# Kernel optimization log

Measured on AMD Instinct MI355X. Metric: run time of the kernel, lower is better.

The kernel has to match this reference:

```python
import jax, jax.numpy as jnp
import numpy as np

D_MODEL = 1024
HEADS = 16
HEAD_DIM = D_MODEL // HEADS


def setup_inputs() -> dict:
    key = jax.random.key(0)
    ks = jax.random.split(key, 6)
    B, S, D = 2, 2048, D_MODEL
    scale = 1.0 / np.sqrt(D)
    x = jax.random.normal(ks[0], (B, S, D), dtype=jnp.float32)
    mask = jax.random.randint(ks[1], (B, S), 0, 2, dtype=jnp.int32)
    Wq = jax.random.normal(ks[2], (D, D), dtype=jnp.float32) * scale
    Wk = jax.random.normal(ks[3], (D, D), dtype=jnp.float32) * scale
    Wv = jax.random.normal(ks[4], (D, D), dtype=jnp.float32) * scale
    Wp = jax.random.normal(ks[5], (D, D), dtype=jnp.float32) * scale
    zb = jnp.zeros((D,), dtype=jnp.float32)
    return {"x": x, "mask": mask, "Wq": Wq, "bq": zb, "Wk": Wk, "bk": zb,
            "Wv": Wv, "bv": zb, "Wp": Wp, "bp": zb}


def reference(x, mask, Wq, bq, Wk, bk, Wv, bv, Wp, bp):
    B, S, D = x.shape
    H, Dh = HEADS, HEAD_DIM

    def split_heads(t):  # [B,S,D] -> [B,H,S,Dh]
        return t.reshape(B, S, H, Dh).transpose(0, 2, 1, 3)

    q = split_heads(x @ Wq + bq)
    k = split_heads(x @ Wk + bk)
    v = split_heads(x @ Wv + bv)

    att = jnp.einsum('bhqd,bhkd->bhqk', q, k) / jnp.sqrt(jnp.float32(Dh))
    # key-padding mask: [B,S] -> [B,1,1,S]; masked positions -> -inf
    m = (mask[:, None, None, :] != 0)
    att = jnp.where(m, att, -jnp.inf)
    att = jax.nn.softmax(att, axis=-1)
    # rows that were fully masked produce NaN -> zero them (masked_fill(isnan, 0))
    att = jnp.where(jnp.isnan(att), 0.0, att)

    y = jnp.einsum('bhqk,bhkd->bhqd', att, v)  # [B,H,S,Dh]
    y = y.transpose(0, 2, 1, 3).reshape(B, S, D)
    return y @ Wp + bp
```

## Files before the change

kernel.cpp:

```cpp
#include <hip/hip_runtime.h>
#include <math.h>

#define D_MODEL 1024
#define HEADS 16
#define HEAD_DIM 64
#define SEQ 2048
#define BATCH 2
#define KVT 64
#define QTILE 128
#define SCALE_Q 0.18033688f

typedef __attribute__((ext_vector_type(8))) short bf16x8;
typedef __attribute__((ext_vector_type(4))) float f32x4;

__device__ __forceinline__ short f2bf(float f) {
    union { float f; unsigned u; } v; v.f = f;
    unsigned r = (v.u + 0x7FFFu + ((v.u >> 16) & 1u)) >> 16;
    return (short)r;
}

__device__ __forceinline__ unsigned cvt_pk_bf16(float lo, float hi) {
    unsigned r;
    asm("v_cvt_pk_bf16_f32 %0, %1, %2" : "=v"(r) : "v"(lo), "v"(hi));
    return r;
}

__device__ __forceinline__ float fexp2(float x) {
    float r;
    asm("v_exp_f32 %0, %1" : "=v"(r) : "v"(x));
    return r;
}

__global__ __launch_bounds__(256) void prep(
    const float* __restrict__ x, const float* __restrict__ Wq,
    const float* __restrict__ Wk, const float* __restrict__ Wv,
    const float* __restrict__ Wp, const int* __restrict__ mask,
    short* __restrict__ xb, short* __restrict__ Wqkvt,
    short* __restrict__ Wpt, float* __restrict__ maskf) {
    __shared__ float t[32][33];
    const int bid = blockIdx.x;
    if (bid < 2048) {
        const int i = bid * 256 + threadIdx.x;
        float4 a = ((const float4*)x)[2 * i];
        float4 b = ((const float4*)x)[2 * i + 1];
        short r[8] = {f2bf(a.x), f2bf(a.y), f2bf(a.z), f2bf(a.w),
                      f2bf(b.x), f2bf(b.y), f2bf(b.z), f2bf(b.w)};
        *(uint4*)(xb + 8 * i) = *(uint4*)r;
    } else if (bid < 6144) {
        const int tt = bid - 2048;
        const int z = tt >> 10;
        const int rem = tt & 1023;
        const float* W = z == 0 ? Wq : z == 1 ? Wk : z == 2 ? Wv : Wp;
        short* dst = (z < 3) ? Wqkvt + (size_t)z * 1024 * 1024 : Wpt;
        const int n0 = (rem & 31) * 32, k0 = (rem >> 5) * 32;
        const int tx = threadIdx.x & 31, ty = threadIdx.x >> 5;
#pragma unroll
        for (int j = 0; j < 4; ++j)
            t[ty + j * 8][tx] = W[(size_t)(k0 + ty + j * 8) * 1024 + n0 + tx];
        __syncthreads();
#pragma unroll
        for (int j = 0; j < 4; ++j) {
            const int n = ty + j * 8;
            dst[(size_t)(n0 + n) * 1024 + k0 + tx] = f2bf(t[tx][n]);
        }
    } else {
        const int i = (bid - 6144) * 256 + threadIdx.x;
        maskf[i] = mask[i] ? 0.f : -INFINITY;
    }
}

template <int MODE>
__global__ __launch_bounds__(256) void mfma_gemm(
    const short* __restrict__ A, const short* __restrict__ Bt,
    const float* __restrict__ b0, const float* __restrict__ b1,
    const float* __restrict__ b2, float* __restrict__ outf,
    short* __restrict__ o0, short* __restrict__ o1, short* __restrict__ o2,
    int M, int N, int K) {
    __shared__ short As[2 * 128 * 32];
    __shared__ short Bs[2 * 128 * 32];

    const int tid = threadIdx.x;
    const int wave = tid >> 6, lane = tid & 63;
    const int l15 = lane & 15, lhi = lane >> 4;
    const int wm = wave >> 1, wn = wave & 1;

    const int nwgx = gridDim.x;
    const int nwg = nwgx * gridDim.y;
    const int lin = blockIdx.y * nwgx + blockIdx.x;
    const int swz = (lin & 7) * (nwg >> 3) + (lin >> 3);
    const int bm0 = (swz / nwgx) * 128, bn0 = (swz % nwgx) * 128;

    f32x4 acc[4][4];
#pragma unroll
    for (int m = 0; m < 4; ++m)
#pragma unroll
        for (int n = 0; n < 4; ++n) acc[m][n] = (f32x4){0.f, 0.f, 0.f, 0.f};

#define STAGE_G(buf, kt_)                                                         \
    {                                                                             \
        const int k0 = (kt_) * 32;                                                \
        _Pragma("unroll") for (int p = 0; p < 2; ++p) {                           \
            const int o = (wave * 2 + p) * 64 + lane;                             \
            const int r = o >> 2;                                                 \
            const int gs = (o & 3) ^ ((r >> 1) & 3);                              \
            __builtin_amdgcn_global_load_lds(                                     \
                (const __attribute__((address_space(1))) void*)(                  \
                    A + (size_t)(bm0 + r) * K + k0 + gs * 8),                     \
                (__attribute__((address_space(3))) void*)(                        \
                    As + (size_t)(buf) * 4096 + (wave * 2 + p) * 512),            \
                16, 0, 0);                                                        \
            __builtin_amdgcn_global_load_lds(                                     \
                (const __attribute__((address_space(1))) void*)(                  \
                    Bt + (size_t)(bn0 + r) * K + k0 + gs * 8),                    \
                (__attribute__((address_space(3))) void*)(                        \
                    Bs + (size_t)(buf) * 4096 + (wave * 2 + p) * 512),            \
                16, 0, 0);                                                        \
        }                                                                         \
    }

    const int NT = K / 32;
    STAGE_G(0, 0);
    __syncthreads();
    for (int kt = 0; kt < NT; ++kt) {
        const int cur = kt & 1;
        if (kt + 1 < NT) STAGE_G((kt + 1) & 1, kt + 1);
        bf16x8 af[4], bf[4];
        const int sg = (lhi ^ ((l15 >> 1) & 3)) * 16;
#pragma unroll
        for (int m = 0; m < 4; ++m)
            af[m] = *(const bf16x8*)((char*)As + cur * 8192 +
                                     (wm * 64 + m * 16 + l15) * 64 + sg);
#pragma unroll
        for (int n = 0; n < 4; ++n)
            bf[n] = *(const bf16x8*)((char*)Bs + cur * 8192 +
                                     (wn * 64 + n * 16 + l15) * 64 + sg);
        __builtin_amdgcn_s_setprio(1);
#pragma unroll
        for (int m = 0; m < 4; ++m)
#pragma unroll
            for (int n = 0; n < 4; ++n)
                acc[m][n] = __builtin_amdgcn_mfma_f32_16x16x32_bf16(af[m], bf[n], acc[m][n], 0, 0, 0);
        __builtin_amdgcn_s_setprio(0);
        __syncthreads();
    }
#undef STAGE_G

    const int which = (MODE == 1) ? (bn0 >> 10) : 0;
#pragma unroll
    for (int m = 0; m < 4; ++m) {
#pragma unroll
        for (int n = 0; n < 4; ++n) {
            const int col = bn0 + wn * 64 + n * 16 + l15;
            if (MODE == 0) {
#pragma unroll
                for (int rr = 0; rr < 4; ++rr) {
                    const int row = bm0 + wm * 64 + m * 16 + lhi * 4 + rr;
                    outf[(size_t)row * N + col] = acc[m][n][rr] + b0[col];
                }
            } else {
                const int cc = col & 1023;
                const int h = cc >> 6, dh = cc & 63;
                const int row0 = bm0 + wm * 64 + m * 16 + lhi * 4;
                const int b = row0 >> 11, s0 = row0 & (SEQ - 1);
                if (which == 2) {
                    const float bias = b2[cc];
                    uint2 w;
                    w.x = cvt_pk_bf16(acc[m][n][0] + bias, acc[m][n][1] + bias);
                    w.y = cvt_pk_bf16(acc[m][n][2] + bias, acc[m][n][3] + bias);
                    *(uint2*)(o2 + ((size_t)(b * HEADS + h) * HEAD_DIM + dh) * SEQ + s0) = w;
                } else {
                    const float bias = (which == 0 ? b0 : b1)[cc];
                    short* dst = which == 0 ? o0 : o1;
#pragma unroll
                    for (int rr = 0; rr < 4; ++rr) {
                        float v = acc[m][n][rr] + bias;
                        if (which == 0) v *= SCALE_Q;
                        dst[(((size_t)(b * HEADS + h)) * SEQ + s0 + rr) * HEAD_DIM + dh] = f2bf(v);
                    }
                }
            }
        }
    }
}

__global__ __launch_bounds__(256, 2) void flash_attn(
    const short* __restrict__ Q, const short* __restrict__ K,
    const short* __restrict__ Vt, const float* __restrict__ maskf,
    short* __restrict__ Y) {
    __shared__ unsigned char kt[2][KVT * 128];
    __shared__ unsigned char vt[2][HEAD_DIM * 128];
    __shared__ unsigned char pb[4][32 * 128];

    const int tid = threadIdx.x;
    const int wave = tid >> 6;
    const int lane = tid & 63;
    const int l15 = lane & 15;
    const int lhi = lane >> 4;

    const int nwg = gridDim.x;
    const int wg = blockIdx.x;
    const int swz = (wg & 7) * (nwg >> 3) + (wg >> 3);
    const int qt = swz & 15;
    const int bh = swz >> 4;
    const int b = bh >> 4;

    const int q0 = qt * QTILE + wave * 32;

    bf16x8 qf[2][2];
#pragma unroll
    for (int qi = 0; qi < 2; ++qi) {
        const short* Qp = Q + ((size_t)bh * SEQ + q0 + 16 * qi + l15) * HEAD_DIM;
        qf[qi][0] = *(const bf16x8*)(Qp + 8 * lhi);
        qf[qi][1] = *(const bf16x8*)(Qp + 8 * lhi + 32);
    }

    const unsigned char* Kb8 = (const unsigned char*)(K + (size_t)bh * SEQ * HEAD_DIM);
    const unsigned char* Vb8 = (const unsigned char*)(Vt + (size_t)bh * HEAD_DIM * SEQ);
    const float* mb = maskf + b * SEQ;

#define STAGE(buf, kvi)                                                            \
    {                                                                              \
        const unsigned char* kbase = Kb8 + (size_t)(kvi) * KVT * 128;              \
        const unsigned char* vbase = Vb8 + (size_t)(kvi) * 128;                    \
        _Pragma("unroll") for (int p = 0; p < 2; ++p) {                            \
            const int o = (wave * 2 + p) * 64 + lane;                              \
            const int row = o >> 3;                                                \
            const int inner = (o & 7) * 16;                                        \
            const int src = inner ^ ((row & 7) << 4);                              \
            __builtin_amdgcn_global_load_lds(                                      \
                (const __attribute__((address_space(1))) void*)(                   \
                    kbase + row * 128 + src),                                      \
                (__attribute__((address_space(3))) void*)(                         \
                    &kt[buf][(wave * 2 + p) * 1024]),                              \
                16, 0, 0);                                                         \
            __builtin_amdgcn_global_load_lds(                                      \
                (const __attribute__((address_space(1))) void*)(                   \
                    vbase + (size_t)row * (SEQ * 2) + src),                        \
                (__attribute__((address_space(3))) void*)(                         \
                    &vt[buf][(wave * 2 + p) * 1024]),                              \
                16, 0, 0);                                                         \
        }                                                                          \
    }

    f32x4 accO[2][4];
    float lrow[2] = {0.f, 0.f};
#pragma unroll
    for (int qi = 0; qi < 2; ++qi)
#pragma unroll
        for (int i = 0; i < 4; ++i) accO[qi][i] = (f32x4){0.f, 0.f, 0.f, 0.f};

    STAGE(0, 0);
    __syncthreads();

    for (int kv = 0; kv < SEQ / KVT; ++kv) {
        const int cur = kv & 1;
        if (kv + 1 < SEQ / KVT) STAGE((kv + 1) & 1, kv + 1);

        const int k0 = kv * KVT;

        f32x4 accS[2][4];
#pragma unroll
        for (int qi = 0; qi < 2; ++qi)
#pragma unroll
            for (int nt = 0; nt < 4; ++nt) accS[qi][nt] = (f32x4){0.f, 0.f, 0.f, 0.f};
#pragma unroll
        for (int c = 0; c < 2; ++c) {
            bf16x8 kf[4];
#pragma unroll
            for (int nt = 0; nt < 4; ++nt) {
                const int key = l15 + 16 * nt;
                kf[nt] = *(const bf16x8*)(kt[cur] + key * 128 +
                                          ((16 * lhi + 64 * c) ^ ((key & 7) << 4)));
            }
            __builtin_amdgcn_s_setprio(1);
#pragma unroll
            for (int qi = 0; qi < 2; ++qi)
#pragma unroll
                for (int nt = 0; nt < 4; ++nt)
                    accS[qi][nt] = __builtin_amdgcn_mfma_f32_16x16x32_bf16(
                        kf[nt], qf[qi][c], accS[qi][nt], 0, 0, 0);
            __builtin_amdgcn_s_setprio(0);
        }

        f32x4 ma[4];
#pragma unroll
        for (int nt = 0; nt < 4; ++nt)
            ma[nt] = *(const f32x4*)(mb + k0 + 16 * nt + 4 * lhi);

#pragma unroll
        for (int qi = 0; qi < 2; ++qi) {
#pragma unroll
            for (int nt = 0; nt < 4; ++nt) {
                f32x4 p;
#pragma unroll
                for (int r = 0; r < 4; ++r) {
                    p[r] = fexp2(accS[qi][nt][r] + ma[nt][r]);
                    lrow[qi] += p[r];
                }
                uint2 w;
                w.x = cvt_pk_bf16(p[0], p[1]);
                w.y = cvt_pk_bf16(p[2], p[3]);
                *(uint2*)(pb[wave] + (l15 + 16 * qi) * 128 +
                          ((32 * nt + 8 * lhi) ^ (l15 << 3))) = w;
            }
        }

#pragma unroll
        for (int c = 0; c < 2; ++c) {
            bf16x8 pf[2];
#pragma unroll
            for (int qi = 0; qi < 2; ++qi) {
                union { bf16x8 v; uint2 u[2]; } pfu;
                pfu.u[0] = *(const uint2*)(pb[wave] + (l15 + 16 * qi) * 128 +
                                           ((16 * lhi + 64 * c) ^ (l15 << 3)));
                pfu.u[1] = *(const uint2*)(pb[wave] + (l15 + 16 * qi) * 128 +
                                           ((16 * lhi + 64 * c + 8) ^ (l15 << 3)));
                pf[qi] = pfu.v;
            }
            bf16x8 vf[4];
#pragma unroll
            for (int d = 0; d < 4; ++d) {
                const int dh = l15 + 16 * d;
                vf[d] = *(const bf16x8*)(vt[cur] + dh * 128 +
                                         ((16 * lhi + 64 * c) ^ ((dh & 7) << 4)));
            }
            __builtin_amdgcn_s_setprio(1);
#pragma unroll
            for (int qi = 0; qi < 2; ++qi)
#pragma unroll
                for (int d = 0; d < 4; ++d)
                    accO[qi][d] = __builtin_amdgcn_mfma_f32_16x16x32_bf16(
                        vf[d], pf[qi], accO[qi][d], 0, 0, 0);
            __builtin_amdgcn_s_setprio(0);
        }
        __syncthreads();
    }
#undef STAGE

#pragma unroll
    for (int qi = 0; qi < 2; ++qi) {
        float rs = lrow[qi];
        rs += __shfl_xor(rs, 16);
        rs += __shfl_xor(rs, 32);
        const float inv = (rs > 0.f) ? 1.f / rs : 0.f;
        const int qg = q0 + 16 * qi + l15;
        short* Yp = Y + ((size_t)b * SEQ + qg) * D_MODEL + (bh & 15) * HEAD_DIM;
#pragma unroll
        for (int d = 0; d < 4; ++d) {
            uint2 w;
            w.x = cvt_pk_bf16(accO[qi][d][0] * inv, accO[qi][d][1] * inv);
            w.y = cvt_pk_bf16(accO[qi][d][2] * inv, accO[qi][d][3] * inv);
            *(uint2*)(Yp + 16 * d + 4 * lhi) = w;
        }
    }
}

extern "C" void kernel_launch(void* const* d_in, const int* in_sizes, int n_in,
                              void* d_out, int out_size, void* d_ws, size_t ws_size,
                              hipStream_t stream) {
    const float* x    = (const float*)d_in[0];
    const int*   mask = (const int*)  d_in[1];
    const float* Wq   = (const float*)d_in[2];
    const float* bq   = (const float*)d_in[3];
    const float* Wk   = (const float*)d_in[4];
    const float* bk   = (const float*)d_in[5];
    const float* Wv   = (const float*)d_in[6];
    const float* bv   = (const float*)d_in[7];
    const float* Wp   = (const float*)d_in[8];
    const float* bp   = (const float*)d_in[9];
    float* out = (float*)d_out;

    short* ws    = (short*)d_ws;
    short* xb    = ws;
    short* Wqkvt = xb + ((size_t)4 << 20);
    short* Wpt   = Wqkvt + ((size_t)3 << 20);
    short* Qb    = Wpt + ((size_t)1 << 20);
    short* Kb    = Qb + ((size_t)4 << 20);
    short* Vtb   = Kb + ((size_t)4 << 20);
    short* Yb    = Vtb + ((size_t)4 << 20);
    float* maskf = (float*)(Yb + ((size_t)4 << 20));

    const int M = BATCH * SEQ;

    prep<<<dim3(6160), 256, 0, stream>>>(x, Wq, Wk, Wv, Wp, mask,
                                         xb, Wqkvt, Wpt, maskf);

    mfma_gemm<1><<<dim3(3 * D_MODEL / 128, M / 128), 256, 0, stream>>>(
        xb, Wqkvt, bq, bk, bv, nullptr, Qb, Kb, Vtb, M, 3 * D_MODEL, D_MODEL);

    flash_attn<<<dim3(BATCH * HEADS * (SEQ / QTILE)), 256, 0, stream>>>(Qb, Kb, Vtb, maskf, Yb);

    mfma_gemm<0><<<dim3(D_MODEL / 128, M / 128), 256, 0, stream>>>(
        Yb, Wpt, bp, bp, bp, out, nullptr, nullptr, nullptr, M, D_MODEL, D_MODEL);
}
```

Before: 123.7 us.

## Split attention KV range in two and merge partial outputs in a new kernel

Splits each query tile's key/value loop into two halves run by separate workgroups, doubling the grid. Each writes unnormalized bf16 partial outputs and row sums, and a new merge kernel adds them and normalizes. It also halves the per-wave P scratch buffer by interleaving the P·V matmul per query subtile, and raises launch bounds to allow 4 blocks per CU. The aim is more parallelism and occupancy, at the cost of an extra kernel launch, extra global traffic and bf16 rounding of unnormalized partials.

After: 170.0 us. 1.37x slower.

```diff
diff --git a/kernel.cpp b/kernel.cpp
--- a/kernel.cpp
+++ b/kernel.cpp
@@ -8,6 +8,7 @@
 #define BATCH 2
 #define KVT 64
 #define QTILE 128
+#define NSPLIT 2
 #define SCALE_Q 0.18033688f
 
 typedef __attribute__((ext_vector_type(8))) short bf16x8;
@@ -29,6 +30,13 @@
     float r;
     asm("v_exp_f32 %0, %1" : "=v"(r) : "v"(x));
     return r;
+}
+
+__device__ __forceinline__ float bflo(unsigned u) {
+    union { unsigned x; float f; } v; v.x = u << 16; return v.f;
+}
+__device__ __forceinline__ float bfhi(unsigned u) {
+    union { unsigned x; float f; } v; v.x = u & 0xffff0000u; return v.f;
 }
 
 __global__ __launch_bounds__(256) void prep(
@@ -183,13 +191,14 @@
     }
 }
 
-__global__ __launch_bounds__(256, 2) void flash_attn(
+__global__ __launch_bounds__(256, 4) void flash_attn(
     const short* __restrict__ Q, const short* __restrict__ K,
     const short* __restrict__ Vt, const float* __restrict__ maskf,
-    short* __restrict__ Y) {
+    short* __restrict__ O0, short* __restrict__ O1,
+    float* __restrict__ l0, float* __restrict__ l1) {
     __shared__ unsigned char kt[2][KVT * 128];
     __shared__ unsigned char vt[2][HEAD_DIM * 128];
-    __shared__ unsigned char pb[4][32 * 128];
+    __shared__ unsigned char pb[4][16 * 128];
 
     const int tid = threadIdx.x;
     const int wave = tid >> 6;
@@ -200,8 +209,9 @@
     const int nwg = gridDim.x;
     const int wg = blockIdx.x;
     const int swz = (wg & 7) * (nwg >> 3) + (wg >> 3);
-    const int qt = swz & 15;
-    const int bh = swz >> 4;
+    const int split = swz & 1;
+    const int qt = (swz >> 1) & 15;
+    const int bh = swz >> 5;
     const int b = bh >> 4;
 
     const int q0 = qt * QTILE + wave * 32;
@@ -249,12 +259,15 @@
 #pragma unroll
         for (int i = 0; i < 4; ++i) accO[qi][i] = (f32x4){0.f, 0.f, 0.f, 0.f};
 
-    STAGE(0, 0);
+    const int kv0 = split * (SEQ / KVT / NSPLIT);
+    const int kv1 = kv0 + (SEQ / KVT / NSPLIT);
+
+    STAGE(0, kv0);
     __syncthreads();
 
-    for (int kv = 0; kv < SEQ / KVT; ++kv) {
+    for (int kv = kv0; kv < kv1; ++kv) {
         const int cur = kv & 1;
-        if (kv + 1 < SEQ / KVT) STAGE((kv + 1) & 1, kv + 1);
+        if (kv + 1 < kv1) STAGE((kv + 1) & 1, kv + 1);
 
         const int k0 = kv * KVT;
 
@@ -300,59 +313,80 @@
                 uint2 w;
                 w.x = cvt_pk_bf16(p[0], p[1]);
                 w.y = cvt_pk_bf16(p[2], p[3]);
-                *(uint2*)(pb[wave] + (l15 + 16 * qi) * 128 +
-                          ((32 * nt + 8 * lhi) ^ (l15 << 3))) = w;
+                *(uint2*)(pb[wave] + l15 * 128 + ((32 * nt + 8 * lhi) ^ (l15 << 3))) = w;
+            }
+#pragma unroll
+            for (int c = 0; c < 2; ++c) {
+                union { bf16x8 v; uint2 u[2]; } pfu;
+                pfu.u[0] = *(const uint2*)(pb[wave] + l15 * 128 +
+                                           ((16 * lhi + 64 * c) ^ (l15 << 3)));
+                pfu.u[1] = *(const uint2*)(pb[wave] + l15 * 128 +
+                                           ((16 * lhi + 64 * c + 8) ^ (l15 << 3)));
+                const bf16x8 pf = pfu.v;
+                bf16x8 vf[4];
+#pragma unroll
+                for (int d = 0; d < 4; ++d) {
+                    const int dh = l15 + 16 * d;
+                    vf[d] = *(const bf16x8*)(vt[cur] + dh * 128 +
+                                             ((16 * lhi + 64 * c) ^ ((dh & 7) << 4)));
+                }
+                __builtin_amdgcn_s_setprio(1);
+#pragma unroll
+                for (int d = 0; d < 4; ++d)
+                    accO[qi][d] = __builtin_amdgcn_mfma_f32_16x16x32_bf16(
+                        vf[d], pf, accO[qi][d], 0, 0, 0);
+                __builtin_amdgcn_s_setprio(0);
             }
         }
-
-#pragma unroll
-        for (int c = 0; c < 2; ++c) {
-            bf16x8 pf[2];
-#pragma unroll
-            for (int qi = 0; qi < 2; ++qi) {
-                union { bf16x8 v; uint2 u[2]; } pfu;
-                pfu.u[0] = *(const uint2*)(pb[wave] + (l15 + 16 * qi) * 128 +
-                                           ((16 * lhi + 64 * c) ^ (l15 << 3)));
-                pfu.u[1] = *(const uint2*)(pb[wave] + (l15 + 16 * qi) * 128 +
-                                           ((16 * lhi + 64 * c + 8) ^ (l15 << 3)));
-                pf[qi] = pfu.v;
-            }
-            bf16x8 vf[4];
-#pragma unroll
-            for (int d = 0; d < 4; ++d) {
-                const int dh = l15 + 16 * d;
-                vf[d] = *(const bf16x8*)(vt[cur] + dh * 128 +
-                                         ((16 * lhi + 64 * c) ^ ((dh & 7) << 4)));
-            }
-            __builtin_amdgcn_s_setprio(1);
-#pragma unroll
-            for (int qi = 0; qi < 2; ++qi)
-#pragma unroll
-                for (int d = 0; d < 4; ++d)
-                    accO[qi][d] = __builtin_amdgcn_mfma_f32_16x16x32_bf16(
-                        vf[d], pf[qi], accO[qi][d], 0, 0, 0);
-            __builtin_amdgcn_s_setprio(0);
-        }
         __syncthreads();
     }
 #undef STAGE
 
+    short* Op = split ? O1 : O0;
+    float* lp = split ? l1 : l0;
 #pragma unroll
     for (int qi = 0; qi < 2; ++qi) {
         float rs = lrow[qi];
         rs += __shfl_xor(rs, 16);
         rs += __shfl_xor(rs, 32);
-        const float inv = (rs > 0.f) ? 1.f / rs : 0.f;
         const int qg = q0 + 16 * qi + l15;
-        short* Yp = Y + ((size_t)b * SEQ + qg) * D_MODEL + (bh & 15) * HEAD_DIM;
+        if (lhi == 0) lp[(size_t)bh * SEQ + qg] = rs;
+        short* Yp = Op + ((size_t)b * SEQ + qg) * D_MODEL + (bh & 15) * HEAD_DIM;
 #pragma unroll
         for (int d = 0; d < 4; ++d) {
             uint2 w;
-            w.x = cvt_pk_bf16(accO[qi][d][0] * inv, accO[qi][d][1] * inv);
-            w.y = cvt_pk_bf16(accO[qi][d][2] * inv, accO[qi][d][3] * inv);
+            w.x = cvt_pk_bf16(accO[qi][d][0], accO[qi][d][1]);
+            w.y = cvt_pk_bf16(accO[qi][d][2], accO[qi][d][3]);
             *(uint2*)(Yp + 16 * d + 4 * lhi) = w;
         }
     }
+}
+
+__global__ __launch_bounds__(256) void merge_o(
+    const short* __restrict__ O0, const short* __restrict__ O1,
+    const float* __restrict__ l0, const float* __restrict__ l1,
+    short* __restrict__ Yb) {
+    const int i = blockIdx.x * 256 + threadIdx.x;
+    const size_t e = (size_t)i * 8;
+    const int row = (int)(e >> 10);
+    const int d = (int)(e & 1023);
+    const int h = d >> 6;
+    const int b = row >> 11;
+    const int q = row & (SEQ - 1);
+    const size_t li = ((size_t)(b * HEADS + h)) * SEQ + q;
+    const float l = l0[li] + l1[li];
+    const float inv = (l > 0.f) ? 1.f / l : 0.f;
+    const uint2 a0 = *(const uint2*)(O0 + e);
+    const uint2 a1 = *(const uint2*)(O0 + e + 4);
+    const uint2 c0 = *(const uint2*)(O1 + e);
+    const uint2 c1 = *(const uint2*)(O1 + e + 4);
+    uint2 r0, r1;
+    r0.x = cvt_pk_bf16((bflo(a0.x) + bflo(c0.x)) * inv, (bfhi(a0.x) + bfhi(c0.x)) * inv);
+    r0.y = cvt_pk_bf16((bflo(a0.y) + bflo(c0.y)) * inv, (bfhi(a0.y) + bfhi(c0.y)) * inv);
+    r1.x = cvt_pk_bf16((bflo(a1.x) + bflo(c1.x)) * inv, (bfhi(a1.x) + bfhi(c1.x)) * inv);
+    r1.y = cvt_pk_bf16((bflo(a1.y) + bflo(c1.y)) * inv, (bfhi(a1.y) + bfhi(c1.y)) * inv);
+    *(uint2*)(Yb + e) = r0;
+    *(uint2*)(Yb + e + 4) = r1;
 }
 
 extern "C" void kernel_launch(void* const* d_in, const int* in_sizes, int n_in,
@@ -379,6 +413,10 @@
     short* Vtb   = Kb + ((size_t)4 << 20);
     short* Yb    = Vtb + ((size_t)4 << 20);
     float* maskf = (float*)(Yb + ((size_t)4 << 20));
+    short* Op0   = (short*)(maskf + 4096);
+    short* Op1   = Op0 + ((size_t)4 << 20);
+    float* lp0   = (float*)(Op1 + ((size_t)4 << 20));
+    float* lp1   = lp0 + ((size_t)BATCH * HEADS * SEQ);
 
     const int M = BATCH * SEQ;
 
@@ -388,7 +426,10 @@
     mfma_gemm<1><<<dim3(3 * D_MODEL / 128, M / 128), 256, 0, stream>>>(
         xb, Wqkvt, bq, bk, bv, nullptr, Qb, Kb, Vtb, M, 3 * D_MODEL, D_MODEL);
 
-    flash_attn<<<dim3(BATCH * HEADS * (SEQ / QTILE)), 256, 0, stream>>>(Qb, Kb, Vtb, maskf, Yb);
+    flash_attn<<<dim3(BATCH * HEADS * (SEQ / QTILE) * NSPLIT), 256, 0, stream>>>(
+        Qb, Kb, Vtb, maskf, Op0, Op1, lp0, lp1);
+
+    merge_o<<<dim3(M * D_MODEL / 8 / 256), 256, 0, stream>>>(Op0, Op1, lp0, lp1, Yb);
 
     mfma_gemm<0><<<dim3(D_MODEL / 128, M / 128), 256, 0, stream>>>(
         Yb, Wpt, bp, bp, bp, out, nullptr, nullptr, nullptr, M, D_MODEL, D_MODEL);
```
